# Kernel optimization log

Hardware: AMD Instinct MI355X
Metric: run time of the kernel (lower is better)

The kernel has to match this reference:

```python
import jax, jax.numpy as jnp
import numpy as np

N = 50000
E = 500000
R = 8
IN_DIM = 128
HID = 128
NUM_CLASSES = 16
NUM_GRAPHS = 64


def setup_inputs() -> dict:
    key = jax.random.key(0)
    ks = jax.random.split(key, 12)
    x = jax.random.normal(ks[0], (N, IN_DIM), dtype=jnp.float32)
    edge_index = jax.random.randint(ks[1], (2, E), 0, N)
    edge_type = jax.random.randint(ks[2], (E,), 0, R)
    batch = jnp.sort(jax.random.randint(ks[3], (N,), 0, NUM_GRAPHS))
    s = 1.0 / np.sqrt(IN_DIM)
    W1 = jax.random.uniform(ks[4], (R, IN_DIM, HID), minval=-s, maxval=s, dtype=jnp.float32)
    root1 = jax.random.uniform(ks[5], (IN_DIM, HID), minval=-s, maxval=s, dtype=jnp.float32)
    b1 = jnp.zeros((HID,), jnp.float32)
    s2 = 1.0 / np.sqrt(HID)
    W2 = jax.random.uniform(ks[6], (R, HID, HID), minval=-s2, maxval=s2, dtype=jnp.float32)
    root2 = jax.random.uniform(ks[7], (HID, HID), minval=-s2, maxval=s2, dtype=jnp.float32)
    b2 = jnp.zeros((HID,), jnp.float32)
    linW = jax.random.uniform(ks[8], (HID, NUM_CLASSES), minval=-s2, maxval=s2, dtype=jnp.float32)
    linb = jnp.zeros((NUM_CLASSES,), jnp.float32)
    return {"x": x, "edge_index": edge_index, "edge_type": edge_type, "batch": batch,
            "W1": W1, "root1": root1, "b1": b1, "W2": W2, "root2": root2, "b2": b2,
            "linW": linW, "linb": linb}


def rgcn_conv(x, src, dst, rel, W, root, b):
    # Per-relation transform of ALL nodes once: [R, N, H] (avoids per-edge weight gather)
    xW = jnp.einsum('nd,rdh->rnh', x, W)
    msg = xW[rel, src]                      # [E, H] gather per edge
    # PyG RGCNConv default aggr='mean': mean over neighbors per (dst, relation)
    seg = dst * R + rel                     # composite segment id
    cnt = jax.ops.segment_sum(jnp.ones((msg.shape[0],), msg.dtype), seg, num_segments=N * R)
    norm = 1.0 / jnp.maximum(cnt, 1.0)
    msg = msg * norm[seg][:, None]
    agg = jax.ops.segment_sum(msg, dst, num_segments=N)  # sum over relations folds in
    return agg + x @ root + b


def global_mean_pool(x, batch):
    sums = jax.ops.segment_sum(x, batch, num_segments=NUM_GRAPHS)
    cnt = jax.ops.segment_sum(jnp.ones((x.shape[0],), x.dtype), batch, num_segments=NUM_GRAPHS)
    return sums / jnp.maximum(cnt, 1.0)[:, None]


def reference(x, edge_index, edge_type, batch, W1, root1, b1, W2, root2, b2, linW, linb):
    src, dst = edge_index[0], edge_index[1]
    h = jax.nn.relu(rgcn_conv(x, src, dst, edge_type, W1, root1, b1))
    h = jax.nn.relu(rgcn_conv(h, src, dst, edge_type, W2, root2, b2))
    pooled = global_mean_pool(h, batch)     # [G, HID]
    return pooled @ linW + linb             # [G, NUM_CLASSES]
```

## Files before the change

### kernel.cpp

```cpp
#include <hip/hip_runtime.h>
#include <hip/hip_bf16.h>
#include <stdint.h>

#define N_NODES 50000
#define N_EDGES 500000
#define R_REL 8
#define HID 128
#define KIN 128
#define KOUT 1152
#define N8 400000
#define NPAD 50048
#define NUM_GRAPHS 64
#define NUM_CLASSES 16

typedef __attribute__((ext_vector_type(8))) short bf16x8;
typedef __attribute__((ext_vector_type(4))) float f32x4;

__device__ __forceinline__ uint16_t f2bf(float f) {
  uint32_t u = __float_as_uint(f);
  u += 0x7FFFu + ((u >> 16) & 1u);
  return (uint16_t)(u >> 16);
}
__device__ __forceinline__ float bf2f(uint32_t b) {
  return __uint_as_float(b << 16);
}
__device__ __forceinline__ uint32_t pack2bf(float a, float b) {
  return (uint32_t)f2bf(a) | ((uint32_t)f2bf(b) << 16);
}

#define HIST_B 1954
#define BND_B 196
#define PW_B 576
__global__ __launch_bounds__(256) void k_prep(const int* __restrict__ ei, const int* __restrict__ et,
                                              int* __restrict__ deg8,
                                              const int* __restrict__ batch,
                                              int* __restrict__ gs, int* __restrict__ ge,
                                              const float* __restrict__ W1, const float* __restrict__ root1,
                                              uint16_t* __restrict__ Wf1,
                                              const float* __restrict__ W2, const float* __restrict__ root2,
                                              uint16_t* __restrict__ Wf2) {
  int b = blockIdx.x;
  if (b < HIST_B) {
    int i = b * 256 + threadIdx.x;
    if (i < N_EDGES) atomicAdd(&deg8[ei[N_EDGES + i] * R_REL + et[i]], 1);
    return;
  }
  b -= HIST_B;
  if (b < BND_B) {
    int i = b * 256 + threadIdx.x;
    if (i < N_NODES) {
      int g = batch[i];
      if (i == 0) gs[g] = 0;
      else { int pg = batch[i - 1]; if (pg != g) { ge[pg] = i; gs[g] = i; } }
      if (i == N_NODES - 1) ge[g] = N_NODES;
    }
    return;
  }
  b -= BND_B;
  {
    const float* W    = (b < PW_B) ? W1 : W2;
    const float* root = (b < PW_B) ? root1 : root2;
    uint16_t*    Wf   = (b < PW_B) ? Wf1 : Wf2;
    int idx = (b % PW_B) * 256 + threadIdx.x;
    int e = idx & 7, L = (idx >> 3) & 63, f = idx >> 9;
    int quad = L >> 4, l16 = L & 15;
    int kc = f & 3, nt = (f >> 2) & 7, s = f >> 5;
    int k = kc * 32 + quad * 8 + e;
    int no = nt * 16 + l16;
    float v = (s < R_REL) ? W[((size_t)s * KIN + k) * HID + no] : root[(size_t)k * HID + no];
    Wf[idx] = f2bf(v);
  }
}

__global__ __launch_bounds__(256) void k_scan1(const int* __restrict__ deg8, int* __restrict__ offs8,
                                               int* __restrict__ bsum) {
  __shared__ int sh[256];
  int t = threadIdx.x;
  int base = blockIdx.x * 1024 + t * 4;
  int v[4]; int s = 0;
  #pragma unroll
  for (int i = 0; i < 4; ++i) { int idx = base + i; v[i] = (idx < N8) ? deg8[idx] : 0; s += v[i]; }
  sh[t] = s;
  __syncthreads();
  for (int d = 1; d < 256; d <<= 1) {
    int add = (t >= d) ? sh[t - d] : 0;
    __syncthreads();
    sh[t] += add;
    __syncthreads();
  }
  int run = sh[t] - s;
  if (t == 255) bsum[blockIdx.x] = sh[255];
  #pragma unroll
  for (int i = 0; i < 4; ++i) { int idx = base + i; if (idx < N8) offs8[idx] = run; run += v[i]; }
}

__global__ __launch_bounds__(512) void k_scan2(int* __restrict__ bsum, int nb) {
  __shared__ int sh[512];
  int t = threadIdx.x;
  int v = (t < nb) ? bsum[t] : 0;
  sh[t] = v;
  __syncthreads();
  for (int d = 1; d < 512; d <<= 1) {
    int add = (t >= d) ? sh[t - d] : 0;
    __syncthreads();
    sh[t] += add;
    __syncthreads();
  }
  if (t < nb) bsum[t] = sh[t] - v;
}

__global__ __launch_bounds__(256) void k_scan3(int* __restrict__ offs8, int* __restrict__ nxt,
                                               const int* __restrict__ bsum) {
  int i = blockIdx.x * 256 + threadIdx.x;
  if (i < N8) {
    int o = offs8[i] + bsum[i >> 10];
    offs8[i] = o;
    nxt[i] = o;
  }
  if (i == 0) offs8[N8] = N_EDGES;
}

__global__ __launch_bounds__(256) void k_scatter(const int* __restrict__ ei, const int* __restrict__ et,
                                                 const int* __restrict__ deg8, int* __restrict__ nxt,
                                                 uint32_t* __restrict__ epack, float* __restrict__ wgt) {
  int i = blockIdx.x * 256 + threadIdx.x;
  if (i < N_EDGES) {
    int rel = et[i];
    int key = ei[N_EDGES + i] * R_REL + rel;
    int p = atomicAdd(&nxt[key], 1);
    epack[p] = (uint32_t)ei[i] | ((uint32_t)rel << 16);
    wgt[p] = 1.0f / (float)deg8[key];
  }
}

template<bool IN_BF16>
__global__ __launch_bounds__(64) void k_gemmY(const void* __restrict__ in,
                                              const uint16_t* __restrict__ Wf,
                                              uint16_t* __restrict__ Y) {
  int L = threadIdx.x;
  int quad = L >> 4, l16 = L & 15;
  int blockM = blockIdx.x * 64;

  bf16x8 af[4][4];
  #pragma unroll
  for (int i = 0; i < 4; ++i) {
    int row = blockM + i * 16 + l16;
    bool valid = row < N_NODES;
    #pragma unroll
    for (int kc = 0; kc < 4; ++kc) {
      if (IN_BF16) {
        uint4 v = {0u, 0u, 0u, 0u};
        if (valid) v = *(const uint4*)((const uint16_t*)in + (size_t)row * KIN + kc * 32 + quad * 8);
        union { uint4 u; bf16x8 b; } cv; cv.u = v;
        af[i][kc] = cv.b;
      } else {
        float4 a = {0.f,0.f,0.f,0.f}, c = {0.f,0.f,0.f,0.f};
        if (valid) {
          const float* p = (const float*)in + (size_t)row * KIN + kc * 32 + quad * 8;
          a = *(const float4*)p;
          c = *(const float4*)(p + 4);
        }
        bf16x8 r;
        r[0] = (short)f2bf(a.x); r[1] = (short)f2bf(a.y); r[2] = (short)f2bf(a.z); r[3] = (short)f2bf(a.w);
        r[4] = (short)f2bf(c.x); r[5] = (short)f2bf(c.y); r[6] = (short)f2bf(c.z); r[7] = (short)f2bf(c.w);
        af[i][kc] = r;
      }
    }
  }

  #pragma unroll 1
  for (int s = 0; s < 9; ++s) {
    f32x4 acc[4][8];
    #pragma unroll
    for (int i = 0; i < 4; ++i)
      #pragma unroll
      for (int nt = 0; nt < 8; ++nt) acc[i][nt] = (f32x4){0.f, 0.f, 0.f, 0.f};
    #pragma unroll
    for (int kc = 0; kc < 4; ++kc) {
      bf16x8 bfr[8];
      #pragma unroll
      for (int nt = 0; nt < 8; ++nt) {
        int f = (s * 8 + nt) * 4 + kc;
        bfr[nt] = *(const bf16x8*)(Wf + (size_t)f * 512 + L * 8);
      }
      #pragma unroll
      for (int i = 0; i < 4; ++i)
        #pragma unroll
        for (int nt = 0; nt < 8; ++nt)
          acc[i][nt] = __builtin_amdgcn_mfma_f32_16x16x32_bf16(af[i][kc], bfr[nt], acc[i][nt], 0, 0, 0);
    }
    #pragma unroll
    for (int i = 0; i < 4; ++i) {
      #pragma unroll
      for (int nt = 0; nt < 8; ++nt) {
        int col = s * 128 + nt * 16 + l16;
        #pragma unroll
        for (int rg = 0; rg < 4; ++rg) {
          int row = blockM + i * 16 + quad * 4 + rg;
          Y[(size_t)row * KOUT + col] = f2bf(acc[i][nt][rg]);
        }
      }
    }
  }
}

template<bool OUT_BF16>
__global__ __launch_bounds__(256) void k_msg(const uint16_t* __restrict__ Y,
                                             const uint32_t* __restrict__ epack,
                                             const float* __restrict__ wgt,
                                             const int* __restrict__ offs8,
                                             const float* __restrict__ bias,
                                             void* __restrict__ hout) {
  int n = (blockIdx.x * 256 + threadIdx.x) >> 6;
  n = __builtin_amdgcn_readfirstlane(n);
  int L = threadIdx.x & 63;
  if (n >= N_NODES) return;
  uint32_t rv = *(const uint32_t*)(Y + (size_t)n * KOUT + R_REL * HID + L * 2);
  float ax = bf2f(rv & 0xFFFFu), ay = bf2f(rv >> 16);
  int o0 = offs8[n * R_REL];
  int o8 = offs8[n * R_REL + R_REL];
  for (int g = o0; g < o8; g += 8) {
    int m8 = min(8, o8 - g);
    uint32_t pv[8]; float wv[8]; uint32_t vv[8];
    #pragma unroll
    for (int i = 0; i < 8; ++i) if (i < m8) { pv[i] = epack[g + i]; wv[i] = wgt[g + i]; }
    #pragma unroll
    for (int i = 0; i < 8; ++i) if (i < m8)
      vv[i] = *(const uint32_t*)(Y + (size_t)(pv[i] & 0xFFFFu) * KOUT + (pv[i] >> 16) * HID + L * 2);
    #pragma unroll
    for (int i = 0; i < 8; ++i) if (i < m8) {
      ax += bf2f(vv[i] & 0xFFFFu) * wv[i];
      ay += bf2f(vv[i] >> 16) * wv[i];
    }
  }
  float2 bb = *(const float2*)(bias + L * 2);
  ax = fmaxf(ax + bb.x, 0.f);
  ay = fmaxf(ay + bb.y, 0.f);
  if (OUT_BF16)
    *(uint32_t*)((uint16_t*)hout + (size_t)n * HID + L * 2) = pack2bf(ax, ay);
  else {
    float2 o2 = {ax, ay};
    *(float2*)((float*)hout + (size_t)n * HID + L * 2) = o2;
  }
}

__global__ __launch_bounds__(256) void k_poolpart(const float* __restrict__ h,
                                                  const int* __restrict__ gs, const int* __restrict__ ge,
                                                  float* __restrict__ psum) {
  __shared__ float red[HID];
  int g = blockIdx.x >> 2, p = blockIdx.x & 3;
  int c = threadIdx.x & 127, ph = threadIdx.x >> 7;
  int s = gs[g], e = ge[g];
  int len = e - s;
  int quarter = (len + 3) >> 2;
  int n0 = s + p * quarter;
  int n1 = min(n0 + quarter, e);
  float acc = 0.f;
  for (int n = n0 + ph; n < n1; n += 2) acc += h[(size_t)n * HID + c];
  if (ph == 1) red[c] = acc;
  __syncthreads();
  if (ph == 0 && n0 < n1) atomicAdd(&psum[g * HID + c], acc + red[c]);
}

__global__ __launch_bounds__(1024) void k_final(const float* __restrict__ psum,
                                                const int* __restrict__ gs, const int* __restrict__ ge,
                                                const float* __restrict__ linW, const float* __restrict__ linb,
                                                float* __restrict__ out) {
  int i = threadIdx.x;
  int g = i >> 4, c = i & 15;
  float inv = 1.f / fmaxf((float)(ge[g] - gs[g]), 1.f);
  float s = 0.f;
  #pragma unroll 8
  for (int k = 0; k < HID; ++k) s += psum[g * HID + k] * linW[k * NUM_CLASSES + c];
  out[i] = s * inv + linb[c];
}

extern "C" void kernel_launch(void* const* d_in, const int* in_sizes, int n_in,
                              void* d_out, int out_size, void* d_ws, size_t ws_size,
                              hipStream_t stream) {
  const float* x     = (const float*)d_in[0];
  const int*   ei    = (const int*)d_in[1];
  const int*   et    = (const int*)d_in[2];
  const int*   batch = (const int*)d_in[3];
  const float* W1    = (const float*)d_in[4];
  const float* root1 = (const float*)d_in[5];
  const float* b1    = (const float*)d_in[6];
  const float* W2    = (const float*)d_in[7];
  const float* root2 = (const float*)d_in[8];
  const float* b2    = (const float*)d_in[9];
  const float* linW  = (const float*)d_in[10];
  const float* linb  = (const float*)d_in[11];
  float* out = (float*)d_out;

  char* ws = (char*)d_ws;
  size_t off = 0;
  auto alloc = [&](size_t bytes) -> char* {
    char* p = ws + off;
    off += (bytes + 255) & ~(size_t)255;
    return p;
  };
  int*      deg8  = (int*)alloc((size_t)N8 * 4);
  int*      gb    = (int*)alloc(2 * NUM_GRAPHS * 4);
  float*    psum  = (float*)alloc((size_t)NUM_GRAPHS * HID * 4);
  size_t zbytes = (size_t)N8 * 4 + 512 + (size_t)NUM_GRAPHS * HID * 4;
  int*      gs    = gb;
  int*      ge    = gb + NUM_GRAPHS;
  int*      offs8 = (int*)alloc((size_t)(N8 + 1) * 4);
  int*      nxt   = (int*)alloc((size_t)N8 * 4);
  int*      bsum  = (int*)alloc(512 * 4);
  uint32_t* epack = (uint32_t*)alloc((size_t)N_EDGES * 4);
  float*    wgt   = (float*)alloc((size_t)N_EDGES * 4);
  uint16_t* Wf1   = (uint16_t*)alloc((size_t)KOUT * KIN * 2);
  uint16_t* Wf2   = (uint16_t*)alloc((size_t)KOUT * KIN * 2);
  uint16_t* Y     = (uint16_t*)alloc((size_t)NPAD * KOUT * 2);
  uint16_t* h1b   = (uint16_t*)alloc((size_t)N_NODES * HID * 2);
  float*    h2    = (float*)alloc((size_t)N_NODES * HID * 4);

  hipMemsetAsync(deg8, 0, zbytes, stream);

  int nb = (N8 + 1023) / 1024;
  k_prep<<<HIST_B + BND_B + 2 * PW_B, 256, 0, stream>>>(
      ei, et, deg8, batch, gs, ge, W1, root1, Wf1, W2, root2, Wf2);
  k_scan1<<<nb, 256, 0, stream>>>(deg8, offs8, bsum);
  k_scan2<<<1, 512, 0, stream>>>(bsum, nb);
  k_scan3<<<(N8 + 255) / 256, 256, 0, stream>>>(offs8, nxt, bsum);
  k_scatter<<<(N_EDGES + 255) / 256, 256, 0, stream>>>(ei, et, deg8, nxt, epack, wgt);

  k_gemmY<false><<<NPAD / 64, 64, 0, stream>>>(x, Wf1, Y);
  k_msg<true ><<<N_NODES / 4, 256, 0, stream>>>(Y, epack, wgt, offs8, b1, h1b);
  k_gemmY<true ><<<NPAD / 64, 64, 0, stream>>>(h1b, Wf2, Y);
  k_msg<false><<<N_NODES / 4, 256, 0, stream>>>(Y, epack, wgt, offs8, b2, h2);

  k_poolpart<<<4 * NUM_GRAPHS, 256, 0, stream>>>(h2, gs, ge, psum);
  k_final<<<1, 1024, 0, stream>>>(psum, gs, ge, linW, linb, out);
}
```

Measured before the change: 316.2 us.

## Split GEMM over relation slices, pack Y stores, interleave edge index and weight

The Y-producing GEMM now launches a 2D grid: one block per relation slice and 64-row tile, with four waves of 16 rows each. This replaces a single wave per block looping over nine slices, and is meant to raise occupancy and parallelism. Outputs are written as packed 32-bit bf16 pairs holding columns c and c+64, and the message kernel reads channels L and L+64 to match that permuted layout. The scatter now stores each edge's packed index and normalization weight together as one uint2. The message loop gathers 16 edges per batch instead of 8, which cuts one separate load stream and adds memory-level parallelism at the cost of more registers.

```diff
diff --git a/kernel.cpp b/kernel.cpp
--- a/kernel.cpp
+++ b/kernel.cpp
@@ -122,92 +122,82 @@
 
 __global__ __launch_bounds__(256) void k_scatter(const int* __restrict__ ei, const int* __restrict__ et,
                                                  const int* __restrict__ deg8, int* __restrict__ nxt,
-                                                 uint32_t* __restrict__ epack, float* __restrict__ wgt) {
+                                                 uint2* __restrict__ epw) {
   int i = blockIdx.x * 256 + threadIdx.x;
   if (i < N_EDGES) {
     int rel = et[i];
     int key = ei[N_EDGES + i] * R_REL + rel;
     int p = atomicAdd(&nxt[key], 1);
-    epack[p] = (uint32_t)ei[i] | ((uint32_t)rel << 16);
-    wgt[p] = 1.0f / (float)deg8[key];
+    uint2 v;
+    v.x = (uint32_t)ei[i] | ((uint32_t)rel << 16);
+    v.y = __float_as_uint(1.0f / (float)deg8[key]);
+    epw[p] = v;
   }
 }
 
 template<bool IN_BF16>
-__global__ __launch_bounds__(64) void k_gemmY(const void* __restrict__ in,
-                                              const uint16_t* __restrict__ Wf,
-                                              uint16_t* __restrict__ Y) {
-  int L = threadIdx.x;
+__global__ __launch_bounds__(256) void k_gemmY(const void* __restrict__ in,
+                                               const uint16_t* __restrict__ Wf,
+                                               uint16_t* __restrict__ Y) {
+  int t = threadIdx.x, w = t >> 6, L = t & 63;
   int quad = L >> 4, l16 = L & 15;
-  int blockM = blockIdx.x * 64;
-
-  bf16x8 af[4][4];
-  #pragma unroll
-  for (int i = 0; i < 4; ++i) {
-    int row = blockM + i * 16 + l16;
-    bool valid = row < N_NODES;
-    #pragma unroll
-    for (int kc = 0; kc < 4; ++kc) {
-      if (IN_BF16) {
-        uint4 v = {0u, 0u, 0u, 0u};
-        if (valid) v = *(const uint4*)((const uint16_t*)in + (size_t)row * KIN + kc * 32 + quad * 8);
-        union { uint4 u; bf16x8 b; } cv; cv.u = v;
-        af[i][kc] = cv.b;
-      } else {
-        float4 a = {0.f,0.f,0.f,0.f}, c = {0.f,0.f,0.f,0.f};
-        if (valid) {
-          const float* p = (const float*)in + (size_t)row * KIN + kc * 32 + quad * 8;
-          a = *(const float4*)p;
-          c = *(const float4*)(p + 4);
-        }
-        bf16x8 r;
-        r[0] = (short)f2bf(a.x); r[1] = (short)f2bf(a.y); r[2] = (short)f2bf(a.z); r[3] = (short)f2bf(a.w);
-        r[4] = (short)f2bf(c.x); r[5] = (short)f2bf(c.y); r[6] = (short)f2bf(c.z); r[7] = (short)f2bf(c.w);
-        af[i][kc] = r;
+  int s = blockIdx.x;
+  int rowB = (blockIdx.y * 4 + w) * 16;
+
+  int row = rowB + l16;
+  bool valid = row < N_NODES;
+  bf16x8 af[4];
+  #pragma unroll
+  for (int kc = 0; kc < 4; ++kc) {
+    if (IN_BF16) {
+      uint4 v = {0u, 0u, 0u, 0u};
+      if (valid) v = *(const uint4*)((const uint16_t*)in + (size_t)row * KIN + kc * 32 + quad * 8);
+      union { uint4 u; bf16x8 b; } cv; cv.u = v;
+      af[kc] = cv.b;
+    } else {
+      float4 a = {0.f,0.f,0.f,0.f}, c = {0.f,0.f,0.f,0.f};
+      if (valid) {
+        const float* p = (const float*)in + (size_t)row * KIN + kc * 32 + quad * 8;
+        a = *(const float4*)p;
+        c = *(const float4*)(p + 4);
       }
-    }
-  }
-
-  #pragma unroll 1
-  for (int s = 0; s < 9; ++s) {
-    f32x4 acc[4][8];
-    #pragma unroll
-    for (int i = 0; i < 4; ++i)
-      #pragma unroll
-      for (int nt = 0; nt < 8; ++nt) acc[i][nt] = (f32x4){0.f, 0.f, 0.f, 0.f};
-    #pragma unroll
-    for (int kc = 0; kc < 4; ++kc) {
-      bf16x8 bfr[8];
-      #pragma unroll
-      for (int nt = 0; nt < 8; ++nt) {
-        int f = (s * 8 + nt) * 4 + kc;
-        bfr[nt] = *(const bf16x8*)(Wf + (size_t)f * 512 + L * 8);
-      }
-      #pragma unroll
-      for (int i = 0; i < 4; ++i)
-        #pragma unroll
-        for (int nt = 0; nt < 8; ++nt)
-          acc[i][nt] = __builtin_amdgcn_mfma_f32_16x16x32_bf16(af[i][kc], bfr[nt], acc[i][nt], 0, 0, 0);
-    }
-    #pragma unroll
-    for (int i = 0; i < 4; ++i) {
-      #pragma unroll
-      for (int nt = 0; nt < 8; ++nt) {
-        int col = s * 128 + nt * 16 + l16;
-        #pragma unroll
-        for (int rg = 0; rg < 4; ++rg) {
-          int row = blockM + i * 16 + quad * 4 + rg;
-          Y[(size_t)row * KOUT + col] = f2bf(acc[i][nt][rg]);
-        }
-      }
+      bf16x8 r;
+      r[0] = (short)f2bf(a.x); r[1] = (short)f2bf(a.y); r[2] = (short)f2bf(a.z); r[3] = (short)f2bf(a.w);
+      r[4] = (short)f2bf(c.x); r[5] = (short)f2bf(c.y); r[6] = (short)f2bf(c.z); r[7] = (short)f2bf(c.w);
+      af[kc] = r;
+    }
+  }
+
+  f32x4 acc[8];
+  #pragma unroll
+  for (int nt = 0; nt < 8; ++nt) acc[nt] = (f32x4){0.f, 0.f, 0.f, 0.f};
+  #pragma unroll
+  for (int kc = 0; kc < 4; ++kc) {
+    bf16x8 bfr[8];
+    #pragma unroll
+    for (int nt = 0; nt < 8; ++nt) {
+      int f = (s * 8 + nt) * 4 + kc;
+      bfr[nt] = *(const bf16x8*)(Wf + (size_t)f * 512 + L * 8);
+    }
+    #pragma unroll
+    for (int nt = 0; nt < 8; ++nt)
+      acc[nt] = __builtin_amdgcn_mfma_f32_16x16x32_bf16(af[kc], bfr[nt], acc[nt], 0, 0, 0);
+  }
+  #pragma unroll
+  for (int ntp = 0; ntp < 4; ++ntp) {
+    int wi = ntp * 16 + l16;
+    #pragma unroll
+    for (int rg = 0; rg < 4; ++rg) {
+      int r = rowB + quad * 4 + rg;
+      uint32_t word = pack2bf(acc[ntp][rg], acc[ntp + 4][rg]);
+      *(uint32_t*)(Y + (size_t)r * KOUT + s * HID + wi * 2) = word;
     }
   }
 }
 
 template<bool OUT_BF16>
 __global__ __launch_bounds__(256) void k_msg(const uint16_t* __restrict__ Y,
-                                             const uint32_t* __restrict__ epack,
-                                             const float* __restrict__ wgt,
+                                             const uint2* __restrict__ epw,
                                              const int* __restrict__ offs8,
                                              const float* __restrict__ bias,
                                              void* __restrict__ hout) {
@@ -216,31 +206,35 @@
   int L = threadIdx.x & 63;
   if (n >= N_NODES) return;
   uint32_t rv = *(const uint32_t*)(Y + (size_t)n * KOUT + R_REL * HID + L * 2);
-  float ax = bf2f(rv & 0xFFFFu), ay = bf2f(rv >> 16);
+  float ax = bf2f(rv & 0xFFFFu);
+  float ay = bf2f(rv >> 16);
   int o0 = offs8[n * R_REL];
   int o8 = offs8[n * R_REL + R_REL];
-  for (int g = o0; g < o8; g += 8) {
-    int m8 = min(8, o8 - g);
-    uint32_t pv[8]; float wv[8]; uint32_t vv[8];
-    #pragma unroll
-    for (int i = 0; i < 8; ++i) if (i < m8) { pv[i] = epack[g + i]; wv[i] = wgt[g + i]; }
-    #pragma unroll
-    for (int i = 0; i < 8; ++i) if (i < m8)
-      vv[i] = *(const uint32_t*)(Y + (size_t)(pv[i] & 0xFFFFu) * KOUT + (pv[i] >> 16) * HID + L * 2);
-    #pragma unroll
-    for (int i = 0; i < 8; ++i) if (i < m8) {
-      ax += bf2f(vv[i] & 0xFFFFu) * wv[i];
-      ay += bf2f(vv[i] >> 16) * wv[i];
-    }
-  }
-  float2 bb = *(const float2*)(bias + L * 2);
-  ax = fmaxf(ax + bb.x, 0.f);
-  ay = fmaxf(ay + bb.y, 0.f);
-  if (OUT_BF16)
-    *(uint32_t*)((uint16_t*)hout + (size_t)n * HID + L * 2) = pack2bf(ax, ay);
-  else {
-    float2 o2 = {ax, ay};
-    *(float2*)((float*)hout + (size_t)n * HID + L * 2) = o2;
+  for (int g = o0; g < o8; g += 16) {
+    int m = min(16, o8 - g);
+    uint2 ev[16]; uint32_t vv[16];
+    #pragma unroll
+    for (int i = 0; i < 16; ++i) if (i < m) ev[i] = epw[g + i];
+    #pragma unroll
+    for (int i = 0; i < 16; ++i) if (i < m)
+      vv[i] = *(const uint32_t*)(Y + (size_t)(ev[i].x & 0xFFFFu) * KOUT + (ev[i].x >> 16) * HID + L * 2);
+    #pragma unroll
+    for (int i = 0; i < 16; ++i) if (i < m) {
+      float wv = __uint_as_float(ev[i].y);
+      ax += bf2f(vv[i] & 0xFFFFu) * wv;
+      ay += bf2f(vv[i] >> 16) * wv;
+    }
+  }
+  ax = fmaxf(ax + bias[L], 0.f);
+  ay = fmaxf(ay + bias[L + 64], 0.f);
+  if (OUT_BF16) {
+    uint16_t* hb = (uint16_t*)hout + (size_t)n * HID;
+    hb[L] = f2bf(ax);
+    hb[L + 64] = f2bf(ay);
+  } else {
+    float* hf = (float*)hout + (size_t)n * HID;
+    hf[L] = ax;
+    hf[L + 64] = ay;
   }
 }
 
@@ -308,8 +302,7 @@
   int*      offs8 = (int*)alloc((size_t)(N8 + 1) * 4);
   int*      nxt   = (int*)alloc((size_t)N8 * 4);
   int*      bsum  = (int*)alloc(512 * 4);
-  uint32_t* epack = (uint32_t*)alloc((size_t)N_EDGES * 4);
-  float*    wgt   = (float*)alloc((size_t)N_EDGES * 4);
+  uint2*    epw   = (uint2*)alloc((size_t)N_EDGES * 8);
   uint16_t* Wf1   = (uint16_t*)alloc((size_t)KOUT * KIN * 2);
   uint16_t* Wf2   = (uint16_t*)alloc((size_t)KOUT * KIN * 2);
   uint16_t* Y     = (uint16_t*)alloc((size_t)NPAD * KOUT * 2);
@@ -324,12 +317,12 @@
   k_scan1<<<nb, 256, 0, stream>>>(deg8, offs8, bsum);
   k_scan2<<<1, 512, 0, stream>>>(bsum, nb);
   k_scan3<<<(N8 + 255) / 256, 256, 0, stream>>>(offs8, nxt, bsum);
-  k_scatter<<<(N_EDGES + 255) / 256, 256, 0, stream>>>(ei, et, deg8, nxt, epack, wgt);
-
-  k_gemmY<false><<<NPAD / 64, 64, 0, stream>>>(x, Wf1, Y);
-  k_msg<true ><<<N_NODES / 4, 256, 0, stream>>>(Y, epack, wgt, offs8, b1, h1b);
-  k_gemmY<true ><<<NPAD / 64, 64, 0, stream>>>(h1b, Wf2, Y);
-  k_msg<false><<<N_NODES / 4, 256, 0, stream>>>(Y, epack, wgt, offs8, b2, h2);
+  k_scatter<<<(N_EDGES + 255) / 256, 256, 0, stream>>>(ei, et, deg8, nxt, epw);
+
+  k_gemmY<false><<<dim3(9, NPAD / 64), 256, 0, stream>>>(x, Wf1, Y);
+  k_msg<true ><<<N_NODES / 4, 256, 0, stream>>>(Y, epw, offs8, b1, h1b);
+  k_gemmY<true ><<<dim3(9, NPAD / 64), 256, 0, stream>>>(h1b, Wf2, Y);
+  k_msg<false><<<N_NODES / 4, 256, 0, stream>>>(Y, epw, offs8, b2, h2);
 
   k_poolpart<<<4 * NUM_GRAPHS, 256, 0, stream>>>(h2, gs, ge, psum);
   k_final<<<1, 1024, 0, stream>>>(psum, gs, ge, linW, linb, out);
```

Result: slower. 349.5 us (+10.5%).
